# Performance work log

Measured on AMD Instinct MI355X. Metric: run time of the kernel, lower is better.

The kernel has to match this reference:

```python
import jax, jax.numpy as jnp
import numpy as np

SR = 48000.0


def _lin_interp(x, n):
    # Matches torch F.interpolate(mode='linear', align_corners=False) on last axis.
    T = x.shape[-1]
    pos = (jnp.arange(n, dtype=jnp.float32) + 0.5) * (T / n) - 0.5
    pos = jnp.clip(pos, 0.0, T - 1)
    i0 = jnp.floor(pos).astype(jnp.int32)
    i1 = jnp.minimum(i0 + 1, T - 1)
    w = (pos - i0.astype(jnp.float32)).astype(x.dtype)
    return jnp.take(x, i0, axis=-1) * (1.0 - w) + jnp.take(x, i1, axis=-1) * w


def setup_inputs() -> dict:
    key = jax.random.key(0)
    k1, k2, k3 = jax.random.split(key, 3)
    B, T, N = 16, 250, 100
    harm_amps = jax.random.uniform(k1, (B, T, N), dtype=jnp.float32)
    # realistic fundamental frequencies: 80..480 Hz
    f0_hz = 80.0 + 400.0 * jax.random.uniform(k2, (B, T), dtype=jnp.float32)
    # small inharmonicity coefficients (piano-like): ~0..1e-4
    inh = 1e-4 * jax.random.uniform(k3, (B,), dtype=jnp.float32)
    return {"harm_amps": harm_amps, "f0_hz": f0_hz, "inh": inh, "n_samples": 48000}


def reference(harm_amps, f0_hz, inh, n_samples):
    B, T, N = harm_amps.shape
    # upsample amplitudes (B,N,n_samples) and f0 (B,n_samples)
    a = _lin_interp(jnp.transpose(harm_amps, (0, 2, 1)), n_samples)
    f0_up = _lin_interp(f0_hz, n_samples)
    k = jnp.arange(1, N + 1, dtype=jnp.float32)  # harmonic numbers 1..N
    stretch = jnp.sqrt(1.0 + inh[:, None] * k ** 2)  # (B,N)
    inst_freq = f0_up[:, None, :] * (k[None, :] * stretch)[:, :, None]  # (B,N,n)
    nyq_mask = (inst_freq < SR * 0.45).astype(a.dtype)
    phase = jnp.cumsum(2.0 * jnp.pi * inst_freq / SR, axis=-1)
    signal = jnp.sum(a * nyq_mask * jnp.sin(phase), axis=1, keepdims=True)  # (B,1,n)
    return signal / N
```

## Files before the change

### kernel.cpp

```cpp
#include <hip/hip_runtime.h>
#include <cmath>

#pragma clang fp contract(off)

#define SRF   48000.0f
#define NYQF  21600.0f
constexpr float  TWO_PI_F  = 6.283185307179586476925286766559f;
constexpr double INV_2PI_D = 0.15915494309189533576888376337251;
constexpr float  RC1 = (float)INV_2PI_D;
constexpr float  RC2 = (float)(INV_2PI_D - (double)RC1);
constexpr double INV_SR_D = 1.0 / 48000.0;
constexpr float  DD1 = (float)INV_SR_D;
constexpr float  DD2 = (float)(INV_SR_D - (double)DD1);

__device__ __forceinline__ float hsin_rev(float r) {
#if __has_builtin(__builtin_amdgcn_sinf)
    return __builtin_amdgcn_sinf(r);
#else
    return __sinf(r * TWO_PI_F);
#endif
}

__device__ __forceinline__ float div48000(float t) {
    float h = t * DD1;
    float r = __builtin_fmaf(t, DD1, -h);
    float s = __builtin_fmaf(t, DD2, r);
    return h + s;
}

__device__ __forceinline__ float sin_phase(float ph) {
    float h  = ph * RC1;
    float r  = __builtin_fmaf(ph, RC1, -h);
    float s  = __builtin_fmaf(ph, RC2, r);
    float nn = __builtin_rintf(h);
    float fr = (h - nn) + s;
    return hsin_rev(fr);
}

template <int IDX>
__device__ __forceinline__ float grp4_bcast(float v, int lb) {
#if __has_builtin(__builtin_amdgcn_ds_swizzle)
    constexpr int imm = (IDX << 5) | 0x1C;
    return __int_as_float(__builtin_amdgcn_ds_swizzle(__float_as_int(v), imm));
#else
    return __shfl(v, lb + IDX);
#endif
}

__device__ __forceinline__ float grp8_bcast0(float v, int lane) {
#if __has_builtin(__builtin_amdgcn_ds_swizzle)
    return __int_as_float(__builtin_amdgcn_ds_swizzle(__float_as_int(v), 0x0018));
#else
    return __shfl(v, lane & ~7);
#endif
}

__device__ __forceinline__ float kcval(int k, float ib) {
    float kf = (float)(k + 1);
    float k2 = kf * kf;
    float m  = ib * k2;
    float s1 = 1.0f + m;
    float st = (float)sqrt((double)s1);
    return kf * st;
}

__global__ void __launch_bounds__(256) k_f0up(const float* __restrict__ f0,
        float* __restrict__ f0up, float* __restrict__ out,
        int T, int n, float pf) {
    int j = blockIdx.x * 256 + threadIdx.x;
    int b = blockIdx.y;
    if (j >= n) return;
    float pos = ((float)j + 0.5f);
    pos = pos * pf;
    pos = pos - 0.5f;
    pos = fmaxf(pos, 0.0f);
    pos = fminf(pos, (float)(T - 1));
    int   i0 = (int)pos;
    int   i1 = min(i0 + 1, T - 1);
    float w  = pos - (float)i0;
    float omw = 1.0f - w;
    const float* fb = f0 + b * T;
    f0up[(size_t)b * n + j] = fb[i0] * omw + fb[i1] * w;
    out[(size_t)b * n + j]  = 0.0f;
}

__global__ void __launch_bounds__(256) k_scan4(const float* __restrict__ f0up,
        const float* __restrict__ inh, float* __restrict__ scan4,
        int N, int n) {
    __shared__ float lv[6016];
    const int k   = blockIdx.x;
    const int b   = blockIdx.y;
    const int tid = threadIdx.x;
    const float kc = kcval(k, inh[b]);
    const float4* f4 = (const float4*)(f0up + (size_t)b * n);
    const int len4 = n >> 4;
    const int len5 = n >> 5;

    auto l2of = [&](float4 v) -> float {
        float a0 = div48000(TWO_PI_F * (kc * v.x));
        float a1 = div48000(TWO_PI_F * (kc * v.y));
        float a2 = div48000(TWO_PI_F * (kc * v.z));
        float a3 = div48000(TWO_PI_F * (kc * v.w));
        return (a0 + a1) + (a2 + a3);
    };
    for (int i = tid; i < len4; i += 256) {
        float s01 = l2of(f4[4*i])     + l2of(f4[4*i + 1]);
        float s23 = l2of(f4[4*i + 2]) + l2of(f4[4*i + 3]);
        lv[i] = s01 + s23;
    }
    __syncthreads();

    int offp = 0, lenp = len4, P = 4;
    for (int l = 5; ; ++l) {
        int lenc = lenp >> 1;
        int offc = offp + lenp;
        for (int i = tid; i < lenc; i += 256)
            lv[offc + i] = lv[offp + 2*i] + lv[offp + 2*i + 1];
        __syncthreads();
        P = l;
        if (lenc == 1) break;
        offp = offc; lenp = lenc;
    }
    for (int l = P - 1; l >= 5; --l) {
        int lenl = n >> l;
        int offl = 0;
        for (int m = 4; m < l; ++m) offl += (n >> m);
        int offh = offl + lenl;
        int lenh = n >> (l + 1);
        float*       arr = lv + offl;
        const float* hi  = lv + offh;
        for (int i = tid; i < lenh; i += 256) {
            float v = hi[i];
            int e = 2*i + 2;
            if (e < lenl) arr[e] = v + arr[e];
            arr[2*i + 1] = v;
        }
        __syncthreads();
    }
    float* sp = scan4 + (size_t)(b * N + k) * (len5 + 1);
    if (tid == 0) sp[0] = 0.0f;
    const float* s5 = lv + len4;
    for (int i = tid; i < len5; i += 256) sp[1 + i] = s5[i];
}

__global__ void __launch_bounds__(256) k_synth4(
        const float* __restrict__ harm, const float* __restrict__ f0up,
        const float* __restrict__ inh,  const float* __restrict__ scan4,
        float* __restrict__ out, int B, int T, int N, int n, float pf, int kpg) {
    const int tid  = threadIdx.x;
    const int b    = blockIdx.y;
    const int k0   = blockIdx.z * kpg;
    const int g    = blockIdx.x * 256 + tid;
    const int q    = g >> 2;
    const int c    = g & 3;
    const int NG   = n >> 4;
    const int NG5P = (n >> 5) + 1;
    const int kend = min(k0 + kpg, N);
    const int kact = kend - k0;
    const bool valid = q < NG;
    const bool oddq  = (q & 1) != 0;
    const int  si    = (q >> 1) + (q & 1);

    __shared__ float2 amps[8 * 32];
    __shared__ float  kcs[32];
    __shared__ float  xp[4][256];

    const float ib    = inh[b];
    const float tmaxf = (float)(T - 1);
    for (int i = tid; i < kact; i += 256) kcs[i] = kcval(k0 + i, ib);

    const int j0blk = blockIdx.x * 1024;
    int i0min;
    {
        float p = ((float)j0blk + 0.5f);
        p = p * pf; p = p - 0.5f;
        p = fmaxf(p, 0.0f); p = fminf(p, tmaxf);
        i0min = (int)p;
    }
    for (int idx = tid; idx < 8 * kact; idx += 256) {
        int r = idx / kact, kk = idx - r * kact;
        int r0 = min(i0min + r, T - 1);
        int r1 = min(i0min + r + 1, T - 1);
        float a0 = harm[((size_t)b * T + r0) * N + (k0 + kk)];
        float a1 = harm[((size_t)b * T + r1) * N + (k0 + kk)];
        amps[idx] = make_float2(a0, a1 - a0);
    }
    __syncthreads();

    float u0=0.f,u1=0.f,u2=0.f,u3=0.f;
    float w0=0.f,w1=0.f,w2=0.f,w3=0.f;
    int   a0o=0,a1o=0,a2o=0,a3o=0;
    float acc0=0.f, acc1=0.f, acc2=0.f, acc3=0.f;
    float um = __builtin_inff();
    if (valid) {
        const float4 v = *(const float4*)(f0up + (size_t)b * n + (size_t)q * 16 + c * 4);
        u0=v.x; u1=v.y; u2=v.z; u3=v.w;
        um = fminf(fminf(u0,u1), fminf(u2,u3));
        const int jb = q * 16 + c * 4;
        #pragma unroll
        for (int i = 0; i < 4; ++i) {
            float p = ((float)(jb + i) + 0.5f);
            p = p * pf; p = p - 0.5f;
            p = fmaxf(p, 0.0f); p = fminf(p, tmaxf);
            int i0 = (int)p;
            float wv = p - (float)i0;
            int aoo  = (i0 - i0min) * kact;
            if (i==0){w0=wv;a0o=aoo;}
            else if (i==1){w1=wv;a1o=aoo;}
            else if (i==2){w2=wv;a2o=aoo;}
            else {w3=wv;a3o=aoo;}
        }
    }
    #pragma unroll
    for (int off = 32; off > 0; off >>= 1)
        um = fminf(um, __shfl_xor(um, off));
    const float umin = um;
    const int lane = tid & 63;
    const int lb   = lane & ~3;

    if (valid) {
        const float* s4k = scan4 + (size_t)(b * N + k0) * NG5P;
        float svc = s4k[si];

        for (int k = k0; k < kend; ++k) {
            const int   kk = k - k0;
            const float kc = kcs[kk];
            if (kc * umin >= NYQF) break;
            const float Sv = svc;
            if (k + 1 < kend) {
                const float* nx = s4k + NG5P;
                svc = nx[si];
                s4k = nx;
            }

            float x0 = div48000(TWO_PI_F * (kc * u0));
            float x1 = div48000(TWO_PI_F * (kc * u1));
            float x2 = div48000(TWO_PI_F * (kc * u2));
            float x3 = div48000(TWO_PI_F * (kc * u3));
            float L1p = x0 + x1, L1q = x2 + x3;
            float L2  = L1p + L1q;

            float s0 = grp4_bcast<0>(L2, lb);
            float s1 = grp4_bcast<1>(L2, lb);
            float s2 = grp4_bcast<2>(L2, lb);
            float s3 = grp4_bcast<3>(L2, lb);
            float t01 = s0 + s1;
            float s23 = s2 + s3;
            float L4v = t01 + s23;
            float G1e = Sv + L4v;
            float Gx  = grp8_bcast0(G1e, lane);
            float G0  = oddq ? Gx : Sv;
            float G1  = oddq ? Sv : G1e;

            float b1v = G0 + s0;
            float b2v = G0 + t01;
            float b3v = b2v + s2;
            float base = (c == 0) ? G0  : (c == 1) ? b1v : (c == 2) ? b2v : b3v;
            float bn   = (c == 0) ? b1v : (c == 1) ? b2v : (c == 2) ? b3v : G1;

            float ph0 = base + x0;
            float ph1 = base + L1p;
            float ph2 = ph1 + x2;
            float ph3 = bn;

            {   float t1 = kc * u0;
                if (t1 < NYQF) { float sv = sin_phase(ph0);
                    float2 a = amps[a0o + kk];
                    acc0 = __builtin_fmaf(__builtin_fmaf(w0, a.y, a.x), sv, acc0); } }
            {   float t1 = kc * u1;
                if (t1 < NYQF) { float sv = sin_phase(ph1);
                    float2 a = amps[a1o + kk];
                    acc1 = __builtin_fmaf(__builtin_fmaf(w1, a.y, a.x), sv, acc1); } }
            {   float t1 = kc * u2;
                if (t1 < NYQF) { float sv = sin_phase(ph2);
                    float2 a = amps[a2o + kk];
                    acc2 = __builtin_fmaf(__builtin_fmaf(w2, a.y, a.x), sv, acc2); } }
            {   float t1 = kc * u3;
                if (t1 < NYQF) { float sv = sin_phase(ph3);
                    float2 a = amps[a3o + kk];
                    acc3 = __builtin_fmaf(__builtin_fmaf(w3, a.y, a.x), sv, acc3); } }
        }
    }

    {
        const int wid  = tid >> 6;
        *(float4*)&xp[wid][4 * lane] = make_float4(acc0, acc1, acc2, acc3);
        const float Nf = (float)N;
        const int jb = blockIdx.x * 1024 + wid * 256;
        float* ob = out + (size_t)b * n + jb;
        #pragma unroll
        for (int i = 0; i < 4; ++i) {
            float v  = xp[wid][i * 64 + lane];
            int   jj = jb + i * 64 + lane;
            if (jj < n) atomicAdd(&ob[i * 64 + lane], v / Nf);
        }
    }
}

__global__ void __launch_bounds__(256) k_scan_synth(
        const float* __restrict__ harm, const float* __restrict__ f0up,
        const float* __restrict__ inh,  float* __restrict__ out,
        int B, int T, int N, int n, float pf) {
    extern __shared__ float lv[];
    const int k   = blockIdx.x;
    const int b   = blockIdx.y;
    const int tid = threadIdx.x;
    const float kc = kcval(k, inh[b]);
    const float* fb = f0up + (size_t)b * n;

    auto inc = [&](int j) -> float {
        float u    = fb[j];
        float inst = kc * u;
        float tt   = TWO_PI_F * inst;
        return tt / SRF;
    };

    const int len1 = n >> 1;
    {
        const float4* f4 = (const float4*)fb;
        for (int i = tid; i < (n >> 2); i += 256) {
            float4 u = f4[i];
            float a0 = (TWO_PI_F * (kc * u.x)) / SRF;
            float a1 = (TWO_PI_F * (kc * u.y)) / SRF;
            float a2 = (TWO_PI_F * (kc * u.z)) / SRF;
            float a3 = (TWO_PI_F * (kc * u.w)) / SRF;
            lv[i] = (a0 + a1) + (a2 + a3);
        }
    }
    __syncthreads();
    int offp = 0, lenp = n >> 2, P = 2;
    for (int l = 3; ; ++l) {
        int lenc = lenp >> 1;
        int offc = offp + lenp;
        for (int i = tid; i < lenc; i += 256)
            lv[offc + i] = lv[offp + 2*i] + lv[offp + 2*i + 1];
        __syncthreads();
        P = l;
        if (lenc == 1) break;
        offp = offc; lenp = lenc;
    }
    for (int l = P - 1; l >= 2; --l) {
        int lenl = n >> l;
        int offl = 0;
        for (int m = 2; m < l; ++m) offl += (n >> m);
        float*       arr = lv + offl;
        const float* hi  = lv + offl + lenl;
        int lenh = n >> (l + 1);
        for (int i = tid; i < lenh; i += 256) {
            float v = hi[i];
            int e = 2*i + 2;
            if (e < lenl) arr[e] = v + arr[e];
            arr[2*i + 1] = v;
        }
        __syncthreads();
    }
    const float* scan2 = lv;

    const float  tmaxf = (float)(T - 1);
    const float  invN  = 1.0f / (float)N;
    const float* hb    = harm + (size_t)b * T * N + k;
    float*       ob    = out + (size_t)b * n;

    auto emit = [&](int j, float ph) {
        float u    = fb[j];
        float inst = kc * u;
        if (!(inst < NYQF)) return;
        double pr = (double)ph * INV_2PI_D;
        double fr = pr - rint(pr);
        float  sv = hsin_rev((float)fr);
        float pos = ((float)j + 0.5f);
        pos = pos * pf; pos = pos - 0.5f;
        pos = fmaxf(pos, 0.0f); pos = fminf(pos, tmaxf);
        int   i0 = (int)pos;
        int   i1 = min(i0 + 1, T - 1);
        float w  = pos - (float)i0;
        float a  = hb[(size_t)i0 * N] * (1.0f - w) + hb[(size_t)i1 * N] * w;
        atomicAdd(&ob[j], (a * sv) * invN);
    };

    if (tid == 0) emit(0, inc(0));
    for (int tt = tid; tt < len1; tt += 256) {
        float s1;
        if (tt == 0)      s1 = inc(0) + inc(1);
        else if (tt & 1)  s1 = scan2[(tt - 1) >> 1];
        else              s1 = scan2[(tt >> 1) - 1] + (inc(2*tt) + inc(2*tt + 1));
        emit(2*tt + 1, s1);
        int je = 2*tt + 2;
        if (je < n) emit(je, s1 + inc(je));
    }
}

extern "C" void kernel_launch(void* const* d_in, const int* in_sizes, int n_in,
                              void* d_out, int out_size, void* d_ws, size_t ws_size,
                              hipStream_t stream) {
    const int B = in_sizes[2];
    const int T = in_sizes[1] / B;
    const int N = in_sizes[0] / (B * T);
    const int n = out_size / B;
    const float pf = (float)((double)T / (double)n);

    const float* harm = (const float*)d_in[0];
    const float* f0   = (const float*)d_in[1];
    const float* inh  = (const float*)d_in[2];
    float* out  = (float*)d_out;
    float* f0up = (float*)d_ws;

    const int KZ  = 4;
    const int kpg = (N + KZ - 1) / KZ;
    const int NG  = n / 16;
    const int NG5 = n / 32;
    const size_t needFast = (size_t)B * n * 4 + (size_t)B * N * (NG5 + 1) * 4;
    const bool fast = (ws_size >= needFast) && (n % 32 == 0) && (kpg <= 32);

    k_f0up<<<dim3((n + 255) / 256, B), 256, 0, stream>>>(f0, f0up, out, T, n, pf);

    if (fast) {
        float* scan4 = (float*)((char*)d_ws + (size_t)B * n * 4);
        k_scan4<<<dim3(N, B), 256, 0, stream>>>(f0up, inh, scan4, N, n);
        const int tiles = (NG * 4 + 255) / 256;
        k_synth4<<<dim3(tiles, B, KZ), 256, 0, stream>>>(
            harm, f0up, inh, scan4, out, B, T, N, n, pf, kpg);
    } else {
        const size_t lds_bytes = (size_t)(n / 2) * sizeof(float);
        k_scan_synth<<<dim3(N, B), 256, lds_bytes, stream>>>(
            harm, f0up, inh, out, B, T, N, n, pf);
    }
}
```

Baseline: 136.7 us.

## Fuse f0 upsampling into scan and synth kernels, drop f0up buffer

Removes the separate f0 upsampling kernel on the fast path: the scan kernel and the synth kernel now recompute the linearly interpolated f0 directly from the small f0 array, and the scan kernel also zeroes the output. The scan tree now starts at the 32-sample level, which halves its shared-memory array and drops one reduction level. This saves a kernel launch and the global write and read of the upsampled f0 buffer. In exchange, each of the N scan blocks recomputes the interpolation, adding redundant ALU work and gathered loads.

```diff
diff --git a/kernel.cpp b/kernel.cpp
--- a/kernel.cpp
+++ b/kernel.cpp
@@ -64,54 +64,70 @@
     return kf * st;
 }
 
+__device__ __forceinline__ float f0interp(const float* __restrict__ fb,
+        int j, int T, float pf, float tmaxf) {
+    float pos = ((float)j + 0.5f);
+    pos = pos * pf;
+    pos = pos - 0.5f;
+    pos = fmaxf(pos, 0.0f);
+    pos = fminf(pos, tmaxf);
+    int   i0 = (int)pos;
+    int   i1 = min(i0 + 1, T - 1);
+    float w  = pos - (float)i0;
+    float omw = 1.0f - w;
+    return fb[i0] * omw + fb[i1] * w;
+}
+
 __global__ void __launch_bounds__(256) k_f0up(const float* __restrict__ f0,
         float* __restrict__ f0up, float* __restrict__ out,
         int T, int n, float pf) {
     int j = blockIdx.x * 256 + threadIdx.x;
     int b = blockIdx.y;
     if (j >= n) return;
-    float pos = ((float)j + 0.5f);
-    pos = pos * pf;
-    pos = pos - 0.5f;
-    pos = fmaxf(pos, 0.0f);
-    pos = fminf(pos, (float)(T - 1));
-    int   i0 = (int)pos;
-    int   i1 = min(i0 + 1, T - 1);
-    float w  = pos - (float)i0;
-    float omw = 1.0f - w;
     const float* fb = f0 + b * T;
-    f0up[(size_t)b * n + j] = fb[i0] * omw + fb[i1] * w;
+    f0up[(size_t)b * n + j] = f0interp(fb, j, T, pf, (float)(T - 1));
     out[(size_t)b * n + j]  = 0.0f;
 }
 
-__global__ void __launch_bounds__(256) k_scan4(const float* __restrict__ f0up,
-        const float* __restrict__ inh, float* __restrict__ scan4,
-        int N, int n) {
-    __shared__ float lv[6016];
+__global__ void __launch_bounds__(256) k_scan5(const float* __restrict__ f0,
+        const float* __restrict__ inh, float* __restrict__ scanS,
+        float* __restrict__ outz, int N, int n, int T, float pf) {
+    __shared__ float lv[3008];
     const int k   = blockIdx.x;
     const int b   = blockIdx.y;
     const int tid = threadIdx.x;
     const float kc = kcval(k, inh[b]);
-    const float4* f4 = (const float4*)(f0up + (size_t)b * n);
-    const int len4 = n >> 4;
+    const float* fb = f0 + b * T;
+    const float tmaxf = (float)(T - 1);
     const int len5 = n >> 5;
 
-    auto l2of = [&](float4 v) -> float {
-        float a0 = div48000(TWO_PI_F * (kc * v.x));
-        float a1 = div48000(TWO_PI_F * (kc * v.y));
-        float a2 = div48000(TWO_PI_F * (kc * v.z));
-        float a3 = div48000(TWO_PI_F * (kc * v.w));
+    {
+        const int chunk = (n + N - 1) / N;
+        const int z0 = k * chunk;
+        for (int i = tid; i < chunk; i += 256) {
+            int j = z0 + i;
+            if (j < n) outz[(size_t)b * n + j] = 0.0f;
+        }
+    }
+
+    auto l2of = [&](int jb) -> float {
+        float a0 = div48000(TWO_PI_F * (kc * f0interp(fb, jb + 0, T, pf, tmaxf)));
+        float a1 = div48000(TWO_PI_F * (kc * f0interp(fb, jb + 1, T, pf, tmaxf)));
+        float a2 = div48000(TWO_PI_F * (kc * f0interp(fb, jb + 2, T, pf, tmaxf)));
+        float a3 = div48000(TWO_PI_F * (kc * f0interp(fb, jb + 3, T, pf, tmaxf)));
         return (a0 + a1) + (a2 + a3);
     };
-    for (int i = tid; i < len4; i += 256) {
-        float s01 = l2of(f4[4*i])     + l2of(f4[4*i + 1]);
-        float s23 = l2of(f4[4*i + 2]) + l2of(f4[4*i + 3]);
-        lv[i] = s01 + s23;
-    }
+    auto l4of = [&](int j) -> float {
+        float s01 = l2of(16 * j)     + l2of(16 * j + 4);
+        float s23 = l2of(16 * j + 8) + l2of(16 * j + 12);
+        return s01 + s23;
+    };
+    for (int i = tid; i < len5; i += 256)
+        lv[i] = l4of(2*i) + l4of(2*i + 1);
     __syncthreads();
 
-    int offp = 0, lenp = len4, P = 4;
-    for (int l = 5; ; ++l) {
+    int offp = 0, lenp = len5, P = 5;
+    for (int l = 6; ; ++l) {
         int lenc = lenp >> 1;
         int offc = offp + lenp;
         for (int i = tid; i < lenc; i += 256)
@@ -124,11 +140,10 @@
     for (int l = P - 1; l >= 5; --l) {
         int lenl = n >> l;
         int offl = 0;
-        for (int m = 4; m < l; ++m) offl += (n >> m);
-        int offh = offl + lenl;
+        for (int m = 5; m < l; ++m) offl += (n >> m);
+        float*       arr = lv + offl;
+        const float* hi  = lv + offl + lenl;
         int lenh = n >> (l + 1);
-        float*       arr = lv + offl;
-        const float* hi  = lv + offh;
         for (int i = tid; i < lenh; i += 256) {
             float v = hi[i];
             int e = 2*i + 2;
@@ -137,15 +152,14 @@
         }
         __syncthreads();
     }
-    float* sp = scan4 + (size_t)(b * N + k) * (len5 + 1);
+    float* sp = scanS + (size_t)(b * N + k) * (len5 + 1);
     if (tid == 0) sp[0] = 0.0f;
-    const float* s5 = lv + len4;
-    for (int i = tid; i < len5; i += 256) sp[1 + i] = s5[i];
+    for (int i = tid; i < len5; i += 256) sp[1 + i] = lv[i];
 }
 
 __global__ void __launch_bounds__(256) k_synth4(
-        const float* __restrict__ harm, const float* __restrict__ f0up,
-        const float* __restrict__ inh,  const float* __restrict__ scan4,
+        const float* __restrict__ harm, const float* __restrict__ f0,
+        const float* __restrict__ inh,  const float* __restrict__ scanS,
         float* __restrict__ out, int B, int T, int N, int n, float pf, int kpg) {
     const int tid  = threadIdx.x;
     const int b    = blockIdx.y;
@@ -193,9 +207,7 @@
     float acc0=0.f, acc1=0.f, acc2=0.f, acc3=0.f;
     float um = __builtin_inff();
     if (valid) {
-        const float4 v = *(const float4*)(f0up + (size_t)b * n + (size_t)q * 16 + c * 4);
-        u0=v.x; u1=v.y; u2=v.z; u3=v.w;
-        um = fminf(fminf(u0,u1), fminf(u2,u3));
+        const float* fb = f0 + b * T;
         const int jb = q * 16 + c * 4;
         #pragma unroll
         for (int i = 0; i < 4; ++i) {
@@ -203,13 +215,17 @@
             p = p * pf; p = p - 0.5f;
             p = fmaxf(p, 0.0f); p = fminf(p, tmaxf);
             int i0 = (int)p;
+            int i1 = min(i0 + 1, T - 1);
             float wv = p - (float)i0;
+            float omw = 1.0f - wv;
+            float uv = fb[i0] * omw + fb[i1] * wv;
             int aoo  = (i0 - i0min) * kact;
-            if (i==0){w0=wv;a0o=aoo;}
-            else if (i==1){w1=wv;a1o=aoo;}
-            else if (i==2){w2=wv;a2o=aoo;}
-            else {w3=wv;a3o=aoo;}
-        }
+            if (i==0){u0=uv;w0=wv;a0o=aoo;}
+            else if (i==1){u1=uv;w1=wv;a1o=aoo;}
+            else if (i==2){u2=uv;w2=wv;a2o=aoo;}
+            else {u3=uv;w3=wv;a3o=aoo;}
+        }
+        um = fminf(fminf(u0,u1), fminf(u2,u3));
     }
     #pragma unroll
     for (int off = 32; off > 0; off >>= 1)
@@ -219,7 +235,7 @@
     const int lb   = lane & ~3;
 
     if (valid) {
-        const float* s4k = scan4 + (size_t)(b * N + k0) * NG5P;
+        const float* s4k = scanS + (size_t)(b * N + k0) * NG5P;
         float svc = s4k[si];
 
         for (int k = k0; k < kend; ++k) {
@@ -403,24 +419,23 @@
     const float* f0   = (const float*)d_in[1];
     const float* inh  = (const float*)d_in[2];
     float* out  = (float*)d_out;
-    float* f0up = (float*)d_ws;
 
     const int KZ  = 4;
     const int kpg = (N + KZ - 1) / KZ;
     const int NG  = n / 16;
     const int NG5 = n / 32;
-    const size_t needFast = (size_t)B * n * 4 + (size_t)B * N * (NG5 + 1) * 4;
+    const size_t needFast = (size_t)B * N * (NG5 + 1) * 4;
     const bool fast = (ws_size >= needFast) && (n % 32 == 0) && (kpg <= 32);
 
-    k_f0up<<<dim3((n + 255) / 256, B), 256, 0, stream>>>(f0, f0up, out, T, n, pf);
-
     if (fast) {
-        float* scan4 = (float*)((char*)d_ws + (size_t)B * n * 4);
-        k_scan4<<<dim3(N, B), 256, 0, stream>>>(f0up, inh, scan4, N, n);
+        float* scanS = (float*)d_ws;
+        k_scan5<<<dim3(N, B), 256, 0, stream>>>(f0, inh, scanS, out, N, n, T, pf);
         const int tiles = (NG * 4 + 255) / 256;
         k_synth4<<<dim3(tiles, B, KZ), 256, 0, stream>>>(
-            harm, f0up, inh, scan4, out, B, T, N, n, pf, kpg);
+            harm, f0, inh, scanS, out, B, T, N, n, pf, kpg);
     } else {
+        float* f0up = (float*)d_ws;
+        k_f0up<<<dim3((n + 255) / 256, B), 256, 0, stream>>>(f0, f0up, out, T, n, pf);
         const size_t lds_bytes = (size_t)(n / 2) * sizeof(float);
         k_scan_synth<<<dim3(N, B), 256, lds_bytes, stream>>>(
             harm, f0up, inh, out, B, T, N, n, pf);
```

Measured after the change: 173.3 us. +26.8%, slower.
